# Kernel tuning notes

Measured on AMD Instinct MI355X. Metric: run time of the kernel, lower is better.

The kernel has to match this reference:

```python
import jax, jax.numpy as jnp
import numpy as np

B, T, E = 4, 2048, 1024
H, HS = 16, 64  # num_head, head_size; H*HS == E


def setup_inputs() -> dict:
    key = jax.random.key(0)
    ks = jax.random.split(key, 6)
    scale = 0.02
    x = jax.random.normal(ks[0], (B, T, E), dtype=jnp.float32)
    # per-head K/Q/V projection weights, stacked: [H, HS, E] (torch Linear weight layout)
    Wk = jax.random.normal(ks[1], (H, HS, E), dtype=jnp.float32) * scale
    Wq = jax.random.normal(ks[2], (H, HS, E), dtype=jnp.float32) * scale
    Wv = jax.random.normal(ks[3], (H, HS, E), dtype=jnp.float32) * scale
    Wo = jax.random.normal(ks[4], (E, E), dtype=jnp.float32) * scale  # proj weight [out, in]
    bo = jax.random.normal(ks[5], (E,), dtype=jnp.float32) * scale
    return {"x": x, "Wk": Wk, "Wq": Wq, "Wv": Wv, "Wo": Wo, "bo": bo}


def reference(x, Wk, Wq, Wv, Wo, bo):
    # per-head projections: [B,T,H,HS]
    k = jnp.einsum('bte,hde->bthd', x, Wk)
    q = jnp.einsum('bte,hde->bthd', x, Wq)
    v = jnp.einsum('bte,hde->bthd', x, Wv)
    # NOTE: source computes wei = k @ q^T (scores[t,s] = k_t . q_s), reproduced faithfully
    scores = jnp.einsum('bthd,bshd->bhts', k, q) * (HS ** -0.5)  # [B,H,T,T]
    causal = jnp.tril(jnp.ones((T, T), dtype=bool))
    scores = jnp.where(causal[None, None], scores, jnp.float32(-jnp.inf))
    wei = jax.nn.softmax(scores, axis=-1)
    out = jnp.einsum('bhts,bshd->bthd', wei, v)  # [B,T,H,HS]
    out = out.reshape(B, T, H * HS)  # concat heads (head-major order matches torch.cat)
    return out @ Wo.T + bo
```

## Files before the change

### kernel.cpp

```cpp
#include <hip/hip_runtime.h>
#include <hip/hip_bf16.h>
#include <stdint.h>

typedef __attribute__((ext_vector_type(8))) __bf16 bf16x8;
typedef __attribute__((ext_vector_type(4))) float f32x4;
typedef __attribute__((ext_vector_type(16))) float f32x16;
typedef unsigned short u16;

#define MFMA16(a, b, c) __builtin_amdgcn_mfma_f32_16x16x32_bf16((a), (b), (c), 0, 0, 0)
#define MFMA32(a, b, c) __builtin_amdgcn_mfma_f32_32x32x16_bf16((a), (b), (c), 0, 0, 0)

__device__ __forceinline__ u16 f32_to_bf16_rne(float f) {
  union { float f; uint32_t u; } v; v.f = f;
  uint32_t u = v.u;
  u += 0x7fffu + ((u >> 16) & 1u);
  return (u16)(u >> 16);
}

__device__ __forceinline__ void gl_lds16(const void* g, void* l) {
  __builtin_amdgcn_global_load_lds(
      (const __attribute__((address_space(1))) void*)(uintptr_t)g,
      (__attribute__((address_space(3))) void*)(uintptr_t)l,
      16, 0, 0);
}

__device__ __forceinline__ float fast_exp2(float x) {
#if __has_builtin(__builtin_amdgcn_exp2f)
  return __builtin_amdgcn_exp2f(x);
#else
  return exp2f(x);
#endif
}

__device__ __forceinline__ uint32_t cvt_pk_bf16(float a, float b) {
  uint32_t r;
  asm("v_cvt_pk_bf16_f32 %0, %1, %2" : "=v"(r) : "v"(a), "v"(b));
  return r;
}

__global__ void cast_all_kernel(const float* __restrict__ x, const float* __restrict__ Wk,
                                const float* __restrict__ Wq, const float* __restrict__ Wv,
                                const float* __restrict__ Wo, u16* __restrict__ xb,
                                u16* __restrict__ wqkv, u16* __restrict__ wob) {
  const int i = blockIdx.x * 256 + threadIdx.x;
  const float* src; u16* dst; int off;
  if (i < 2097152)      { src = x;  dst = xb;             off = i; }
  else if (i < 2359296) { src = Wk; dst = wqkv;           off = i - 2097152; }
  else if (i < 2621440) { src = Wq; dst = wqkv + 1048576; off = i - 2359296; }
  else if (i < 2883584) { src = Wv; dst = wqkv + 2097152; off = i - 2621440; }
  else                  { src = Wo; dst = wob;            off = i - 2883584; }
  float4 v = reinterpret_cast<const float4*>(src)[off];
  ushort4 o;
  o.x = f32_to_bf16_rne(v.x);
  o.y = f32_to_bf16_rne(v.y);
  o.z = f32_to_bf16_rne(v.z);
  o.w = f32_to_bf16_rne(v.w);
  reinterpret_cast<ushort4*>(dst)[off] = o;
}

template <int FINAL>
__global__ __launch_bounds__(256, 2) void gemm_bt_kernel(
    const u16* __restrict__ A, const u16* __restrict__ Bt,
    void* __restrict__ Cout, const float* __restrict__ bias, int M, int N, int K) {
  __shared__ __attribute__((aligned(16))) u16 As[128 * 32];
  __shared__ __attribute__((aligned(16))) u16 Bs[128 * 32];
  const int tid = threadIdx.x;
  const int lane = tid & 63;
  const int wid = tid >> 6;
  const int wr = wid >> 1, wc = wid & 1;
  const int m0 = blockIdx.y * 128, n0 = blockIdx.x * 128;

  f32x4 acc[4][4] = {};

  const int sr = lane >> 2;
  const int scc = lane & 3;
  const int sh = (sr ^ (sr >> 2)) & 3;
  const int sc = ((scc ^ sh) << 3);
  const int rl = lane & 15;
  const int rh = (rl ^ (rl >> 2)) & 3;
  const int cpr = (((lane >> 4) ^ rh) << 4);

  for (int k0 = 0; k0 < K; k0 += 32) {
    __syncthreads();
#pragma unroll
    for (int i = 0; i < 2; ++i) {
      const int c = wid * 2 + i;
      const int row = c * 16 + sr;
      gl_lds16(A + (size_t)(m0 + row) * K + k0 + sc, (char*)As + c * 1024);
      gl_lds16(Bt + (size_t)(n0 + row) * K + k0 + sc, (char*)Bs + c * 1024);
    }
    __syncthreads();

    bf16x8 af[4], bf[4];
#pragma unroll
    for (int mi = 0; mi < 4; ++mi)
      af[mi] = *(const bf16x8*)((const char*)As + (wr * 64 + mi * 16 + rl) * 64 + cpr);
#pragma unroll
    for (int ni = 0; ni < 4; ++ni)
      bf[ni] = *(const bf16x8*)((const char*)Bs + (wc * 64 + ni * 16 + rl) * 64 + cpr);
    __builtin_amdgcn_s_setprio(1);
#pragma unroll
    for (int mi = 0; mi < 4; ++mi)
#pragma unroll
      for (int ni = 0; ni < 4; ++ni)
        acc[mi][ni] = MFMA16(af[mi], bf[ni], acc[mi][ni]);
    __builtin_amdgcn_s_setprio(0);
  }

#pragma unroll
  for (int mi = 0; mi < 4; ++mi) {
#pragma unroll
    for (int ni = 0; ni < 4; ++ni) {
      const int row = m0 + wr * 64 + mi * 16 + ((lane >> 4) << 2);
      const int col = n0 + wc * 64 + ni * 16 + (lane & 15);
#pragma unroll
      for (int j = 0; j < 4; ++j) {
        if (FINAL) {
          reinterpret_cast<float*>(Cout)[(size_t)(row + j) * N + col] =
              acc[mi][ni][j] + bias[col];
        } else {
          reinterpret_cast<u16*>(Cout)[(size_t)(row + j) * N + col] =
              f32_to_bf16_rne(acc[mi][ni][j]);
        }
      }
    }
  }
}

#define KQVS 3072
#define SCL 0.18033688011f
#define NEG (-1e30f)

__device__ __forceinline__ void v_load(uint4* vr, const u16* __restrict__ Vsrc,
                                       int s0, int tid) {
#pragma unroll
  for (int it = 0; it < 2; ++it) {
    const int idx = it * 256 + tid;
    const int g = idx & 7, srow = idx >> 3;
    vr[it] = *reinterpret_cast<const uint4*>(Vsrc + (size_t)(s0 + srow) * KQVS + g * 8);
  }
}

__device__ __forceinline__ void vt_write(u16* buf, const uint4* vr, int tid) {
#pragma unroll
  for (int it = 0; it < 2; ++it) {
    const int idx = it * 256 + tid;
    const int g = idx & 7, srow = idx >> 3;
    const u16* pv = reinterpret_cast<const u16*>(&vr[it]);
#pragma unroll
    for (int u = 0; u < 8; ++u) {
      const int ue = (u + g) & 7;
      const int d = g * 8 + ue;
      buf[((srow >> 3) * 64 + d) * 8 + (srow & 7)] = pv[ue];
    }
  }
}

__global__ __launch_bounds__(256, 3) void attn_kernel(
    const u16* __restrict__ KQV, u16* __restrict__ Ob) {
  __shared__ __attribute__((aligned(16))) char smem[32768];

  const int tid = threadIdx.x;
  const int lane = tid & 63;
  const int wv = tid >> 6;
  const int l31 = lane & 31;
  const int hh = lane >> 5;
  const bool lolane = (hh == 0);

  const int idx = blockIdx.x;
  const int ttile = 15 - (idx >> 6);
  const int bhpos = idx & 63;
  const int bh = (bhpos & 7) * 8 + (bhpos >> 3);
  const int b = bh >> 4, head = bh & 15;

  const size_t rbase = (size_t)b * 2048;
  const u16* Kh = KQV + rbase * KQVS + head * 64;
  const u16* Qh = Kh + 1024;
  const u16* Vh = Kh + 2048;
  u16* Oh = Ob + rbase * 1024 + head * 64;

  const int t0 = ttile * 128;
  const int nst = 2 * ttile + 2;
  const int t0w = t0 + wv * 32;
  const int tl = t0w + l31;
  const int rb4 = 4 * hh;

#pragma unroll
  for (int i = 0; i < 4; ++i) {
    const int ch = wv * 4 + i;
    const int cc = ch >> 1;
    const int trow = (ch & 1) * 64 + lane;
    gl_lds16(Kh + (size_t)(t0 + trow) * KQVS + cc * 8, smem + 16384 + ch * 1024);
  }
#pragma unroll
  for (int i = 0; i < 2; ++i) {
    const int ch = wv * 2 + i;
    gl_lds16(Qh + (size_t)lane * KQVS + ch * 8, smem + ch * 1024);
  }
  {
    uint4 vr0[2];
    v_load(vr0, Vh, 0, tid);
    vt_write((u16*)(smem + 8192), vr0, tid);
  }
  __syncthreads();

  bf16x8 kf[4];
  {
    const u16* Ksp = (const u16*)(smem + 16384);
#pragma unroll
    for (int kk = 0; kk < 4; ++kk)
      kf[kk] = *(const bf16x8*)(Ksp + ((kk * 2 + hh) * 128 + wv * 32 + l31) * 8);
  }
  __syncthreads();

  f32x16 oa0 = {}, oa1 = {};
  float l_run = 0.f;

#pragma unroll 1
  for (int st = 0; st < nst; ++st) {
    const int cur = st & 1;
    const int s0 = st * 64;
    const bool pref = (st + 1 < nst);
    uint4 vr[2];
    if (pref) {
      v_load(vr, Vh, s0 + 64, tid);
#pragma unroll
      for (int i = 0; i < 2; ++i) {
        const int ch = wv * 2 + i;
        gl_lds16(Qh + (size_t)(s0 + 64 + lane) * KQVS + ch * 8,
                 smem + (cur ^ 1) * 16384 + ch * 1024);
      }
    }

    const bool active = (s0 <= t0w + 31);
    f32x16 sa0 = {}, sa1 = {};
    if (active) {
      if (pref) {
        asm volatile("s_waitcnt vmcnt(4)" ::: "memory");
      } else {
        asm volatile("s_waitcnt vmcnt(0)" ::: "memory");
      }
      __builtin_amdgcn_sched_barrier(0);

      const u16* qb = (const u16*)(smem + cur * 16384);
      __builtin_amdgcn_s_setprio(1);
#pragma unroll
      for (int kk = 0; kk < 4; ++kk) {
        bf16x8 a0 = *(const bf16x8*)(qb + ((kk * 2 + hh) * 64 + l31) * 8);
        bf16x8 a1 = *(const bf16x8*)(qb + ((kk * 2 + hh) * 64 + 32 + l31) * 8);
        sa0 = MFMA32(a0, kf[kk], sa0);
        sa1 = MFMA32(a1, kf[kk], sa1);
      }
      __builtin_amdgcn_s_setprio(0);

      if (s0 + 63 > t0w) {
#pragma unroll
        for (int r = 0; r < 16; ++r) {
          const int rowloc = (r & 3) + 8 * (r >> 2) + rb4;
          if (s0 + rowloc > tl) sa0[r] = NEG;
          if (s0 + 32 + rowloc > tl) sa1[r] = NEG;
        }
      }

#pragma unroll
      for (int r = 0; r < 16; ++r) {
        sa0[r] = fast_exp2(sa0[r] * SCL);
        sa1[r] = fast_exp2(sa1[r] * SCL);
      }
      float rsA = ((sa0[0] + sa0[1]) + (sa0[2] + sa0[3])) +
                  ((sa0[4] + sa0[5]) + (sa0[6] + sa0[7]));
      float rsB = ((sa0[8] + sa0[9]) + (sa0[10] + sa0[11])) +
                  ((sa0[12] + sa0[13]) + (sa0[14] + sa0[15]));
      float rsC = ((sa1[0] + sa1[1]) + (sa1[2] + sa1[3])) +
                  ((sa1[4] + sa1[5]) + (sa1[6] + sa1[7]));
      float rsD = ((sa1[8] + sa1[9]) + (sa1[10] + sa1[11])) +
                  ((sa1[12] + sa1[13]) + (sa1[14] + sa1[15]));
      float rs = (rsA + rsB) + (rsC + rsD);
      rs += __shfl_xor(rs, 32);
      l_run += rs;
    }

    if (pref) vt_write((u16*)(smem + (cur ^ 1) * 16384 + 8192), vr, tid);

    if (active) {
      const u16* vb = (const u16*)(smem + cur * 16384 + 8192);
      __builtin_amdgcn_s_setprio(1);
#define PV_WINDOW(P, r0, w)                                                   \
  {                                                                           \
    uint32_t dA = cvt_pk_bf16(P[r0 + 0], P[r0 + 1]);                          \
    uint32_t dB = cvt_pk_bf16(P[r0 + 2], P[r0 + 3]);                          \
    uint32_t dC = cvt_pk_bf16(P[r0 + 4], P[r0 + 5]);                          \
    uint32_t dD = cvt_pk_bf16(P[r0 + 6], P[r0 + 7]);                          \
    uint32_t sdA = (uint32_t)__shfl_xor((int)dA, 32);                         \
    uint32_t sdB = (uint32_t)__shfl_xor((int)dB, 32);                         \
    uint32_t sdC = (uint32_t)__shfl_xor((int)dC, 32);                         \
    uint32_t sdD = (uint32_t)__shfl_xor((int)dD, 32);                         \
    union { uint32_t u[4]; bf16x8 v; } af;                                    \
    af.u[0] = lolane ? dA : sdC;                                              \
    af.u[1] = lolane ? dB : sdD;                                              \
    af.u[2] = lolane ? sdA : dC;                                              \
    af.u[3] = lolane ? sdB : dD;                                              \
    bf16x8 bv0 = *(const bf16x8*)(vb + ((2 * (w) + hh) * 64 + l31) * 8);      \
    bf16x8 bv1 = *(const bf16x8*)(vb + ((2 * (w) + hh) * 64 + 32 + l31) * 8); \
    oa0 = MFMA32(af.v, bv0, oa0);                                             \
    oa1 = MFMA32(af.v, bv1, oa1);                                             \
  }
      PV_WINDOW(sa0, 0, 0)
      PV_WINDOW(sa0, 8, 1)
      PV_WINDOW(sa1, 0, 2)
      PV_WINDOW(sa1, 8, 3)
#undef PV_WINDOW
      __builtin_amdgcn_s_setprio(0);
    }

    asm volatile("s_waitcnt lgkmcnt(0)" ::: "memory");
    __builtin_amdgcn_s_barrier();
  }

  {
    const float inv = 1.0f / l_run;
#pragma unroll
    for (int r = 0; r < 16; ++r) {
      const int rowloc = (r & 3) + 8 * (r >> 2) + rb4;
      const float ir = __shfl(inv, rowloc);
      const int trow = t0w + rowloc;
      Oh[(size_t)trow * 1024 + l31] = f32_to_bf16_rne(oa0[r] * ir);
      Oh[(size_t)trow * 1024 + 32 + l31] = f32_to_bf16_rne(oa1[r] * ir);
    }
  }
}

extern "C" void kernel_launch(void* const* d_in, const int* in_sizes, int n_in,
                              void* d_out, int out_size, void* d_ws, size_t ws_size,
                              hipStream_t stream) {
  (void)in_sizes; (void)n_in; (void)out_size; (void)ws_size;
  const float* x  = (const float*)d_in[0];
  const float* Wk = (const float*)d_in[1];
  const float* Wq = (const float*)d_in[2];
  const float* Wv = (const float*)d_in[3];
  const float* Wo = (const float*)d_in[4];
  const float* bo = (const float*)d_in[5];
  float* out = (float*)d_out;

  char* ws = (char*)d_ws;
  u16* xb   = (u16*)(ws);
  u16* kqv  = (u16*)(ws + ((size_t)16 << 20));
  u16* wqkv = (u16*)(ws + ((size_t)64 << 20));
  u16* wob  = (u16*)(ws + ((size_t)70 << 20));

  cast_all_kernel<<<dim3(12288), 256, 0, stream>>>(x, Wk, Wq, Wv, Wo, xb, wqkv, wob);

  gemm_bt_kernel<0><<<dim3(24, 64), 256, 0, stream>>>(xb, wqkv, kqv, nullptr, 8192, 3072, 1024);

  attn_kernel<<<dim3(1024), 256, 0, stream>>>(kqv, xb);

  gemm_bt_kernel<1><<<dim3(8, 64), 256, 0, stream>>>(xb, wob, out, bo, 8192, 1024, 1024);
}
```

Before: 190.9 us.

## Replace QKV projection GEMM with 256x256-tile, 8-wave pipelined LDS kernel

Adds a new GEMM kernel for the QKV projection that uses 256x256 output tiles, 512 threads and 128 KB of double-buffered LDS. Global-to-LDS loads go directly through XOR-swizzled async copies and are interleaved phase by phase with MFMA work, using barriers, vmcnt waits and setprio. Block IDs are remapped to improve L2 locality. The aim is more data reuse per tile and better overlap of memory traffic with compute. The cost is lower occupancy and a grid of only 384 blocks on this problem.

```diff
diff --git a/kernel.cpp b/kernel.cpp
--- a/kernel.cpp
+++ b/kernel.cpp
@@ -123,6 +123,127 @@
               f32_to_bf16_rne(acc[mi][ni][j]);
         }
       }
+    }
+  }
+}
+
+__device__ __forceinline__ void g256_stage(const u16* __restrict__ src, int b0,
+                                           int half, int t, char* region, int K,
+                                           int tid) {
+  char* dst = region + half * 16384;
+  const int w64 = tid & ~63;
+  const int lane = tid & 63;
+#pragma unroll
+  for (int j = 0; j < 2; ++j) {
+    const int gbase = j * 512 + w64;
+    const int gI = gbase + lane;
+    const int r = gI >> 3;
+    const int c = ((gI & 7) ^ (r & 7)) * 8;
+    gl_lds16(src + (size_t)(b0 + half * 128 + r) * K + t * 64 + c,
+             dst + gbase * 16);
+  }
+}
+
+template <int Q, bool LOADB, int VM>
+__device__ __forceinline__ void g256_phase(
+    char* lds, int slot, const u16* __restrict__ A, const u16* __restrict__ Bt,
+    int m0, int n0, int K, int stT, int stHalf, bool stIsB, int stSlot,
+    int wm, int wn, int l15, int l4, int tid,
+    bf16x8 (&bf)[2][4], f32x4 (&acc)[8][4]) {
+  const char* Ab = lds + slot * 65536 + wm * 16384;
+  if (LOADB) {
+    const char* Bb = lds + slot * 65536 + 32768 + (wn >> 1) * 16384;
+#pragma unroll
+    for (int kk = 0; kk < 2; ++kk)
+#pragma unroll
+      for (int ni = 0; ni < 4; ++ni) {
+        const int lr = (wn & 1) * 64 + ni * 16 + l15;
+        bf[kk][ni] = *(const bf16x8*)(Bb + lr * 128 + (((kk * 4 + l4) ^ (lr & 7)) << 4));
+      }
+  }
+  bf16x8 af[2][2];
+#pragma unroll
+  for (int mi = 0; mi < 2; ++mi)
+#pragma unroll
+    for (int kk = 0; kk < 2; ++kk) {
+      const int lr = (Q * 2 + mi) * 16 + l15;
+      af[mi][kk] = *(const bf16x8*)(Ab + lr * 128 + (((kk * 4 + l4) ^ (lr & 7)) << 4));
+    }
+  {
+    const u16* src = stIsB ? Bt : A;
+    const int b0 = stIsB ? n0 : m0;
+    char* region = lds + stSlot * 65536 + (stIsB ? 32768 : 0);
+    g256_stage(src, b0, stHalf, stT, region, K, tid);
+  }
+  if (VM == 4) asm volatile("s_waitcnt vmcnt(4)" ::: "memory");
+  __builtin_amdgcn_s_barrier();
+  __builtin_amdgcn_s_setprio(1);
+#pragma unroll
+  for (int mi = 0; mi < 2; ++mi)
+#pragma unroll
+    for (int ni = 0; ni < 4; ++ni)
+#pragma unroll
+      for (int kk = 0; kk < 2; ++kk)
+        acc[Q * 2 + mi][ni] = MFMA16(af[mi][kk], bf[kk][ni], acc[Q * 2 + mi][ni]);
+  __builtin_amdgcn_s_setprio(0);
+  __builtin_amdgcn_s_barrier();
+}
+
+__global__ __launch_bounds__(512) void gemm256_kernel(
+    const u16* __restrict__ A, const u16* __restrict__ Bt, u16* __restrict__ C,
+    int M, int N, int K) {
+  __shared__ __attribute__((aligned(16))) char lds[131072];
+
+  const int tid = threadIdx.x;
+  const int lane = tid & 63;
+  const int w = tid >> 6;
+  const int wm = w >> 2, wn = w & 3;
+  const int l15 = lane & 15, l4 = lane >> 4;
+
+  const int bid = blockIdx.x;
+  const int wg = (bid & 7) * (gridDim.x >> 3) + (bid >> 3);
+  const int nbx = N >> 8;
+  const int by = wg / nbx, bx = wg - by * nbx;
+  const int m0 = by << 8, n0 = bx << 8;
+
+  f32x4 acc[8][4] = {};
+  bf16x8 bf[2][4];
+
+  g256_stage(A, m0, 0, 0, lds, K, tid);
+  g256_stage(A, m0, 1, 0, lds, K, tid);
+  g256_stage(Bt, n0, 0, 0, lds + 32768, K, tid);
+  g256_stage(Bt, n0, 1, 0, lds + 32768, K, tid);
+  g256_stage(Bt, n0, 0, 1, lds + 65536 + 32768, K, tid);
+  g256_stage(Bt, n0, 1, 1, lds + 65536 + 32768, K, tid);
+  asm volatile("s_waitcnt vmcnt(4)" ::: "memory");
+  __builtin_amdgcn_s_barrier();
+
+  const int KT = K >> 6;
+#pragma unroll 1
+  for (int it = 0; it < (KT >> 1); ++it) {
+    const int t1 = it * 2 + 1;
+    int t2 = it * 2 + 2; if (t2 > KT - 1) t2 = KT - 1;
+    int t3 = it * 2 + 3; if (t3 > KT - 1) t3 = KT - 1;
+    g256_phase<0, true, -1>(lds, 0, A, Bt, m0, n0, K, t1, 0, false, 1, wm, wn, l15, l4, tid, bf, acc);
+    g256_phase<1, false, -1>(lds, 0, A, Bt, m0, n0, K, t1, 1, false, 1, wm, wn, l15, l4, tid, bf, acc);
+    g256_phase<2, false, -1>(lds, 0, A, Bt, m0, n0, K, t2, 0, true, 0, wm, wn, l15, l4, tid, bf, acc);
+    g256_phase<3, false, 4>(lds, 0, A, Bt, m0, n0, K, t2, 1, true, 0, wm, wn, l15, l4, tid, bf, acc);
+    g256_phase<0, true, -1>(lds, 1, A, Bt, m0, n0, K, t2, 0, false, 0, wm, wn, l15, l4, tid, bf, acc);
+    g256_phase<1, false, -1>(lds, 1, A, Bt, m0, n0, K, t2, 1, false, 0, wm, wn, l15, l4, tid, bf, acc);
+    g256_phase<2, false, -1>(lds, 1, A, Bt, m0, n0, K, t3, 0, true, 1, wm, wn, l15, l4, tid, bf, acc);
+    g256_phase<3, false, 4>(lds, 1, A, Bt, m0, n0, K, t3, 1, true, 1, wm, wn, l15, l4, tid, bf, acc);
+  }
+  asm volatile("s_waitcnt vmcnt(0)" ::: "memory");
+
+#pragma unroll
+  for (int mi = 0; mi < 8; ++mi) {
+#pragma unroll
+    for (int ni = 0; ni < 4; ++ni) {
+      const int row = m0 + wm * 128 + mi * 16 + l4 * 4;
+      const int col = n0 + wn * 64 + ni * 16 + l15;
+#pragma unroll
+      for (int j = 0; j < 4; ++j)
+        C[(size_t)(row + j) * N + col] = f32_to_bf16_rne(acc[mi][ni][j]);
     }
   }
 }
@@ -350,7 +471,7 @@
 
   cast_all_kernel<<<dim3(12288), 256, 0, stream>>>(x, Wk, Wq, Wv, Wo, xb, wqkv, wob);
 
-  gemm_bt_kernel<0><<<dim3(24, 64), 256, 0, stream>>>(xb, wqkv, kqv, nullptr, 8192, 3072, 1024);
+  gemm256_kernel<<<dim3(384), 512, 0, stream>>>(xb, wqkv, kqv, 8192, 3072, 1024);
 
   attn_kernel<<<dim3(1024), 256, 0, stream>>>(kqv, xb);
 
```

After: 186.2 us, median of 2. -2.5%, faster.
